# Kernel tuning notes

Hardware: AMD Instinct MI355X
Metric: run time of the kernel (lower is better)

## Reference

```python
import jax, jax.numpy as jnp
import numpy as np

H = 64   # hidden size
V = 29   # vocab / feature size
SOS = 27 # start-token index set to 1 in the initial one-hot


def _cell(x, h, c, Wih, Whh, bih, bhh):
    # PyTorch LSTMCell gate order: i, f, g, o
    g = x @ Wih.T + h @ Whh.T + bih + bhh
    i, f, gg, o = jnp.split(g, 4, axis=-1)
    c = jax.nn.sigmoid(f) * c + jax.nn.sigmoid(i) * jnp.tanh(gg)
    h = jax.nn.sigmoid(o) * jnp.tanh(c)
    return h, c


def setup_inputs() -> dict:
    key = jax.random.key(0)
    ks = iter(jax.random.split(key, 32))
    T, B = 1024, 512
    def p(shape, scale=0.05):
        return jax.random.normal(next(ks), shape, dtype=jnp.float32) * scale
    inp = {"input_seq": jax.random.normal(next(ks), (T, B, V), dtype=jnp.float32)}
    inp.update(
        enc_Wih0=p((4 * H, V)), enc_Whh0=p((4 * H, H)), enc_bih0=p((4 * H,)), enc_bhh0=p((4 * H,)),
        enc_Wih1=p((4 * H, H)), enc_Whh1=p((4 * H, H)), enc_bih1=p((4 * H,)), enc_bhh1=p((4 * H,)),
        d1_Wih=p((4 * H, V)), d1_Whh=p((4 * H, H)), d1_bih=p((4 * H,)), d1_bhh=p((4 * H,)),
        d2_Wih=p((4 * H, H)), d2_Whh=p((4 * H, H)), d2_bih=p((4 * H,)), d2_bhh=p((4 * H,)),
        cls_W=p((V, H)), cls_b=p((V,)),
    )
    return inp


def reference(input_seq, enc_Wih0, enc_Whh0, enc_bih0, enc_bhh0,
              enc_Wih1, enc_Whh1, enc_bih1, enc_bhh1,
              d1_Wih, d1_Whh, d1_bih, d1_bhh,
              d2_Wih, d2_Whh, d2_bih, d2_bhh,
              cls_W, cls_b):
    T, B, _ = input_seq.shape
    dt = input_seq.dtype
    z = jnp.zeros((B, H), dt)

    def layer(x_seq, Wih, Whh, bih, bhh):
        def step(carry, x):
            h, c = _cell(x, carry[0], carry[1], Wih, Whh, bih, bhh)
            return (h, c), h
        (h, c), ys = jax.lax.scan(step, (z, z), x_seq)
        return ys, h, c

    # 2-layer encoder LSTM with zero initial state
    y1, _, _ = layer(input_seq, enc_Wih0, enc_Whh0, enc_bih0, enc_bhh0)
    _, h1, c1 = layer(y1, enc_Wih1, enc_Whh1, enc_bih1, enc_bhh1)  # top-layer final (h, c)

    let0 = jnp.zeros((B, V), dt).at[:, SOS].set(1.0)

    def dec_step(carry, _):
        h1, c1, h2, c2, let = carry
        h1, c1 = _cell(let, h1, c1, d1_Wih, d1_Whh, d1_bih, d1_bhh)
        h2, c2 = _cell(h1, h2, c2, d2_Wih, d2_Whh, d2_bih, d2_bhh)
        pred = h2 @ cls_W.T + cls_b  # [B, V]
        idx = jnp.argmax(pred, axis=-1)  # [B]
        # Faithful to original bug: sets column idx[b] to 1 for ALL rows, for each b
        let = jnp.zeros((B, V), pred.dtype).at[:, idx].set(1.0)
        return (h1, c1, h2, c2, let), pred

    _, outputs = jax.lax.scan(dec_step, (h1, c1, z, z, let0), None, length=T)
    return outputs  # [T, B, V]
```

## Files before the change

kernel.cpp:

```cpp
#include <hip/hip_runtime.h>
#include <math.h>

#define TSTEPS 1024
#define BATCH  512
#define HID    64
#define VOC    29
#define SOS    27
#define MASK29 0x1FFFFFFFu

#define ENC_BLOCKS 256
#define DEC_BLOCKS 256
#define NTHREADS   512

__device__ __forceinline__ float frcp(float x){ return __builtin_amdgcn_rcpf(x); }
__device__ __forceinline__ float sigmf(float x){ return frcp(1.0f + __expf(-x)); }
__device__ __forceinline__ float tanhfast(float x){ return 1.0f - 2.0f*frcp(1.0f + __expf(2.0f*x)); }

__global__ __attribute__((amdgpu_flat_work_group_size(NTHREADS,NTHREADS), amdgpu_waves_per_eu(2,2)))
void enc_kernel(const float* __restrict__ x,
                const float* __restrict__ Wih0, const float* __restrict__ Whh0,
                const float* __restrict__ bih0, const float* __restrict__ bhh0,
                const float* __restrict__ Wih1, const float* __restrict__ Whh1,
                const float* __restrict__ bih1, const float* __restrict__ bhh1,
                float* __restrict__ h1g, float* __restrict__ c1g)
{
  const int tid = threadIdx.x;
  const int b0  = blockIdx.x * 2;
  const bool g0 = tid < 256;
  const int  r  = g0 ? tid : (tid-256);

  __shared__ __align__(16) float xs[2][32];
  __shared__ __align__(16) float h0s[2][HID], h1s[2][HID];
  __shared__ __align__(16) float gA[2][256], gB[2][256];

  float wh[64], w2[64];
  if (g0){
    #pragma unroll
    for (int k=0;k<64;k++) wh[k] = Whh0[r*64+k];
    #pragma unroll
    for (int k=0;k<29;k++) w2[k] = Wih0[r*29+k];
    #pragma unroll
    for (int k=29;k<64;k++) w2[k] = 0.f;
  } else {
    #pragma unroll
    for (int k=0;k<64;k++){ wh[k] = Whh1[r*64+k]; w2[k] = Wih1[r*64+k]; }
  }
  const float bias = g0 ? (bih0[r]+bhh0[r]) : (bih1[r]+bhh1[r]);

  float creg = 0.f;
  if (tid < 128){ int u=tid>>6,k=tid&63; h0s[u][k]=0.f; h1s[u][k]=0.f; }

  const int pidx = tid - 448;
  const bool pf  = (pidx >= 0) && (pidx < 2*VOC);
  const int prow = pf ? (pidx/VOC) : 0;
  const int pcol = pf ? (pidx%VOC) : 0;
  if (pf) xs[prow][pcol] = x[(size_t)(b0+prow)*VOC + pcol];
  __syncthreads();

  for (int t=0;t<=TSTEPS;t++){
    float xv = 0.f;
    if (pf && t+1 < TSTEPS)
      xv = x[(size_t)(t+1)*BATCH*VOC + (size_t)(b0+prow)*VOC + pcol];

    if (g0){
      if (t < TSTEPS){
        #pragma unroll
        for (int u=0;u<2;u++){
          float a0=bias,a1=0.f,a2=0.f,a3=0.f;
          const float4* xv4 = (const float4*)xs[u];
          #pragma unroll
          for (int c=0;c<7;c++){
            float4 q=xv4[c];
            a0=fmaf(q.x,w2[4*c+0],a0); a1=fmaf(q.y,w2[4*c+1],a1);
            a2=fmaf(q.z,w2[4*c+2],a2); a3=fmaf(q.w,w2[4*c+3],a3);
          }
          a0=fmaf(xs[u][28],w2[28],a0);
          const float4* h4=(const float4*)h0s[u];
          #pragma unroll
          for (int c=0;c<16;c++){
            float4 q=h4[c];
            a0=fmaf(q.x,wh[4*c+0],a0); a1=fmaf(q.y,wh[4*c+1],a1);
            a2=fmaf(q.z,wh[4*c+2],a2); a3=fmaf(q.w,wh[4*c+3],a3);
          }
          gA[u][r]=(a0+a1)+(a2+a3);
        }
      }
    } else {
      if (t >= 1){
        #pragma unroll
        for (int u=0;u<2;u++){
          float a0=bias,a1=0.f,a2=0.f,a3=0.f;
          const float4* i4=(const float4*)h0s[u];
          const float4* h4=(const float4*)h1s[u];
          #pragma unroll
          for (int c=0;c<16;c++){
            float4 q=i4[c], w=h4[c];
            a0=fmaf(q.x,w2[4*c+0],a0); a1=fmaf(q.y,w2[4*c+1],a1);
            a2=fmaf(q.z,w2[4*c+2],a2); a3=fmaf(q.w,w2[4*c+3],a3);
            a0=fmaf(w.x,wh[4*c+0],a0); a1=fmaf(w.y,wh[4*c+1],a1);
            a2=fmaf(w.z,wh[4*c+2],a2); a3=fmaf(w.w,wh[4*c+3],a3);
          }
          gB[u][r]=(a0+a1)+(a2+a3);
        }
      }
    }
    __syncthreads();
    if (tid < 128){
      if (t < TSTEPS){
        int u=tid>>6,k=tid&63;
        float ig=gA[u][k],fg=gA[u][64+k],gg=gA[u][128+k],og=gA[u][192+k];
        float c=sigmf(fg)*creg + sigmf(ig)*tanhfast(gg);
        creg=c; h0s[u][k]=sigmf(og)*tanhfast(c);
      }
    } else if (tid < 384){
      if (t >= 1){
        int tt=tid-256,u=tt>>6,k=tt&63;
        float ig=gB[u][k],fg=gB[u][64+k],gg=gB[u][128+k],og=gB[u][192+k];
        float c=sigmf(fg)*creg + sigmf(ig)*tanhfast(gg);
        creg=c; h1s[u][k]=sigmf(og)*tanhfast(c);
      }
    }
    if (pf && t+1 < TSTEPS) xs[prow][pcol] = xv;
    __syncthreads();
  }

  if (tid >= 256 && tid < 384){
    int tt=tid-256,u=tt>>6,k=tt&63;
    h1g[(b0+u)*HID+k]=h1s[u][k];
    c1g[(b0+u)*HID+k]=creg;
  }
}

__global__ __attribute__((amdgpu_flat_work_group_size(NTHREADS,NTHREADS), amdgpu_waves_per_eu(2,2)))
void dec_kernel(const float* __restrict__ h1gp, const float* __restrict__ c1gp,
                const float* __restrict__ W1ih, const float* __restrict__ W1hh,
                const float* __restrict__ b1ih, const float* __restrict__ b1hh,
                const float* __restrict__ W2ih, const float* __restrict__ W2hh,
                const float* __restrict__ b2ih, const float* __restrict__ b2hh,
                const float* __restrict__ clsW, const float* __restrict__ clsb,
                float* __restrict__ out,
                unsigned long long* __restrict__ lvl1)
{
  const int tid  = threadIdx.x;
  const int r    = tid >> 1;
  const int p    = tid & 1;
  const int b0   = blockIdx.x * 2;
  const unsigned grp = blockIdx.x & 15;
  const unsigned idx = blockIdx.x >> 4;

  __shared__ __align__(16) float clsW_s[VOC][68];
  __shared__ __align__(16) float clsb_s[32];
  __shared__ __align__(16) float gl[2][256];
  __shared__ __align__(16) float h1s[2][HID], h2s[2][HID];
  __shared__ unsigned maskLDS;

  for (int i=tid;i<VOC*HID;i+=NTHREADS) clsW_s[i/HID][i%HID] = clsW[i];
  if (tid<VOC) clsb_s[tid]=clsb[tid];

  float w1h[32], w2i[32], w2h[32], wi1c[15];
  #pragma unroll
  for (int k=0;k<32;k++){
    w1h[k]=W1hh[r*HID+32*p+k];
    w2i[k]=W2ih[r*HID+32*p+k];
    w2h[k]=W2hh[r*HID+32*p+k];
  }
  const int cbase = p ? 15 : 0;
  const int cn    = p ? 14 : 15;
  #pragma unroll
  for (int j=0;j<15;j++) wi1c[j] = (j<cn) ? W1ih[r*VOC+cbase+j] : 0.f;
  const float biasg = p ? 0.f : (b1ih[r]+b1hh[r]);
  const float bias2 = p ? 0.f : (b2ih[r]+b2hh[r]);

  float c1reg=0.f, c2reg=0.f;
  if (tid<128){
    int u=tid>>6,k=tid&63;
    h1s[u][k]=h1gp[(b0+u)*HID+k];
    c1reg    =c1gp[(b0+u)*HID+k];
    h2s[u][k]=0.f;
  }
  __syncthreads();

  float hd1[2];
  #pragma unroll
  for (int u=0;u<2;u++){
    float a0=0.f,a1=0.f,a2=0.f,a3=0.f;
    const float4* h4=(const float4*)(h1s[u]+32*p);
    #pragma unroll
    for (int c=0;c<8;c++){
      float4 q=h4[c];
      a0=fmaf(q.x,w1h[4*c+0],a0); a1=fmaf(q.y,w1h[4*c+1],a1);
      a2=fmaf(q.z,w1h[4*c+2],a2); a3=fmaf(q.w,w1h[4*c+3],a3);
    }
    hd1[u]=(a0+a1)+(a2+a3);
  }

  unsigned mask = 1u<<SOS;

  for (int s=0;s<TSTEPS;s++){
    #pragma unroll
    for (int u=0;u<2;u++){
      float it = biasg;
      #pragma unroll
      for (int j=0;j<15;j++)
        it += ((mask>>(cbase+j))&1u) ? wi1c[j] : 0.f;
      float v = it + hd1[u];
      v += __shfl_xor(v,1);
      if (!p) gl[u][r] = v;
    }
    __syncthreads();
    if (tid<128){
      int u=tid>>6,k=tid&63;
      float ig=gl[u][k],fg=gl[u][64+k],gg=gl[u][128+k],og=gl[u][192+k];
      float c=sigmf(fg)*c1reg+sigmf(ig)*tanhfast(gg);
      c1reg=c; h1s[u][k]=sigmf(og)*tanhfast(c);
    }
    __syncthreads();
    #pragma unroll
    for (int u=0;u<2;u++){
      float a0=bias2,a1=0.f,a2=0.f,a3=0.f;
      const float4* i4=(const float4*)(h1s[u]+32*p);
      const float4* h4=(const float4*)(h2s[u]+32*p);
      #pragma unroll
      for (int c=0;c<8;c++){
        float4 q=i4[c], w=h4[c];
        a0=fmaf(q.x,w2i[4*c+0],a0); a1=fmaf(q.y,w2i[4*c+1],a1);
        a2=fmaf(q.z,w2i[4*c+2],a2); a3=fmaf(q.w,w2i[4*c+3],a3);
        a0=fmaf(w.x,w2h[4*c+0],a0); a1=fmaf(w.y,w2h[4*c+1],a1);
        a2=fmaf(w.z,w2h[4*c+2],a2); a3=fmaf(w.w,w2h[4*c+3],a3);
      }
      float v=(a0+a1)+(a2+a3);
      v += __shfl_xor(v,1);
      if (!p) gl[u][r]=v;
    }
    __syncthreads();
    if (tid<128){
      int u=tid>>6,k=tid&63;
      float ig=gl[u][k],fg=gl[u][64+k],gg=gl[u][128+k],og=gl[u][192+k];
      float c=sigmf(fg)*c2reg+sigmf(ig)*tanhfast(gg);
      c2reg=c; h2s[u][k]=sigmf(og)*tanhfast(c);
    }
    __syncthreads();
    if (tid<64){
      int row=tid>>5, v=tid&31;
      float pv = -INFINITY;
      if (v<VOC){
        float a0=clsb_s[v],a1=0.f,a2=0.f,a3=0.f;
        const float4* h4=(const float4*)h2s[row];
        #pragma unroll
        for (int c=0;c<16;c++){
          float4 q=h4[c];
          a0=fmaf(q.x,clsW_s[v][4*c+0],a0); a1=fmaf(q.y,clsW_s[v][4*c+1],a1);
          a2=fmaf(q.z,clsW_s[v][4*c+2],a2); a3=fmaf(q.w,clsW_s[v][4*c+3],a3);
        }
        pv=(a0+a1)+(a2+a3);
        out[((size_t)s*BATCH + (size_t)(b0+row))*VOC + v]=pv;
      }
      int ix=v;
      #pragma unroll
      for (int off=16; off>0; off>>=1){
        float ov=__shfl_xor(pv,off);
        int   oi=__shfl_xor(ix,off);
        if (ov>pv || (ov==pv && oi<ix)){ pv=ov; ix=oi; }
      }
      unsigned bit = 1u<<ix;
      unsigned mb  = bit | __shfl_xor(bit,32);
      if (tid==0 && s+1<TSTEPS)
        __hip_atomic_fetch_or(&lvl1[(size_t)grp*TSTEPS+s],
                              (unsigned long long)mb | (1ULL<<(32+idx)),
                              __ATOMIC_RELAXED, __HIP_MEMORY_SCOPE_AGENT);
    }
    if (s+1<TSTEPS){
      #pragma unroll
      for (int u=0;u<2;u++){
        float a0=0.f,a1=0.f,a2=0.f,a3=0.f;
        const float4* h4=(const float4*)(h1s[u]+32*p);
        #pragma unroll
        for (int c=0;c<8;c++){
          float4 q=h4[c];
          a0=fmaf(q.x,w1h[4*c+0],a0); a1=fmaf(q.y,w1h[4*c+1],a1);
          a2=fmaf(q.z,w1h[4*c+2],a2); a3=fmaf(q.w,w1h[4*c+3],a3);
        }
        hd1[u]=(a0+a1)+(a2+a3);
      }
      if (tid<64){
        while (true){
          unsigned long long u64 = 0;
          if (tid<16)
            u64 = __hip_atomic_load(&lvl1[(size_t)tid*TSTEPS+s],
                                    __ATOMIC_RELAXED, __HIP_MEMORY_SCOPE_AGENT);
          bool ok = (tid>=16) || ((unsigned)(u64>>32) == 0xFFFFu);
          if (__ballot(ok) == ~0ull){
            unsigned m = (tid<16) ? ((unsigned)u64 & MASK29) : 0u;
            m |= __shfl_xor(m,1); m |= __shfl_xor(m,2);
            m |= __shfl_xor(m,4); m |= __shfl_xor(m,8);
            if (tid==0) maskLDS = m;
            break;
          }
        }
      }
      __syncthreads();
      mask = maskLDS;
    }
  }
}

extern "C" void kernel_launch(void* const* d_in, const int* in_sizes, int n_in,
                              void* d_out, int out_size, void* d_ws, size_t ws_size,
                              hipStream_t stream)
{
  const float* x     = (const float*)d_in[0];
  const float* eWih0 = (const float*)d_in[1];
  const float* eWhh0 = (const float*)d_in[2];
  const float* ebih0 = (const float*)d_in[3];
  const float* ebhh0 = (const float*)d_in[4];
  const float* eWih1 = (const float*)d_in[5];
  const float* eWhh1 = (const float*)d_in[6];
  const float* ebih1 = (const float*)d_in[7];
  const float* ebhh1 = (const float*)d_in[8];
  const float* d1Wih = (const float*)d_in[9];
  const float* d1Whh = (const float*)d_in[10];
  const float* d1bih = (const float*)d_in[11];
  const float* d1bhh = (const float*)d_in[12];
  const float* d2Wih = (const float*)d_in[13];
  const float* d2Whh = (const float*)d_in[14];
  const float* d2bih = (const float*)d_in[15];
  const float* d2bhh = (const float*)d_in[16];
  const float* clsW  = (const float*)d_in[17];
  const float* clsb  = (const float*)d_in[18];
  float* out = (float*)d_out;

  float* h1g = (float*)d_ws;
  float* c1g = h1g + BATCH*HID;
  unsigned long long* lvl1 = (unsigned long long*)((char*)d_ws + (size_t)(2*BATCH*HID)*sizeof(float));

  hipMemsetAsync(lvl1, 0, 16*TSTEPS*sizeof(unsigned long long), stream);

  enc_kernel<<<ENC_BLOCKS, NTHREADS, 0, stream>>>(
      x, eWih0,eWhh0,ebih0,ebhh0, eWih1,eWhh1,ebih1,ebhh1, h1g,c1g);

  void* args[] = { (void*)&h1g, (void*)&c1g,
                   (void*)&d1Wih,(void*)&d1Whh,(void*)&d1bih,(void*)&d1bhh,
                   (void*)&d2Wih,(void*)&d2Whh,(void*)&d2bih,(void*)&d2bhh,
                   (void*)&clsW,(void*)&clsb,(void*)&out,(void*)&lvl1 };
  hipLaunchCooperativeKernel((void*)dec_kernel, dim3(DEC_BLOCKS), dim3(NTHREADS),
                             args, 0, stream);
}
```

Before: 5.881 ms.

## Remap decoder threads so gate octets compute cell update via shuffles

Decoder threads are remapped so that the 8 lanes handling one hidden unit hold all four gate rows (i,f,g,o) split in halves. After a pairwise shuffle reduction, lane 0 of each octet gathers the other gates by xor-shuffles and updates the cell directly, which removes the shared gate buffer and two block barriers per step. The h1/h2 shared buffers are double-buffered to avoid read/write hazards, and an s_sleep is added in the spin-wait loop to reduce polling pressure. The cell update now runs on 1 of every 8 lanes and c state is replicated in registers.

```diff
diff --git a/kernel.cpp b/kernel.cpp
--- a/kernel.cpp
+++ b/kernel.cpp
@@ -141,42 +141,43 @@
                 float* __restrict__ out,
                 unsigned long long* __restrict__ lvl1)
 {
-  const int tid  = threadIdx.x;
-  const int r    = tid >> 1;
-  const int p    = tid & 1;
-  const int b0   = blockIdx.x * 2;
+  const int tid = threadIdx.x;
+  const int k   = tid >> 3;
+  const int l   = tid & 7;
+  const int g   = l >> 1;
+  const int p   = l & 1;
+  const int b0  = blockIdx.x * 2;
   const unsigned grp = blockIdx.x & 15;
   const unsigned idx = blockIdx.x >> 4;
+  const int row = g*64 + k;
 
   __shared__ __align__(16) float clsW_s[VOC][68];
   __shared__ __align__(16) float clsb_s[32];
-  __shared__ __align__(16) float gl[2][256];
-  __shared__ __align__(16) float h1s[2][HID], h2s[2][HID];
+  __shared__ __align__(16) float h1s[2][2][HID], h2s[2][2][HID];
   __shared__ unsigned maskLDS;
 
-  for (int i=tid;i<VOC*HID;i+=NTHREADS) clsW_s[i/HID][i%HID] = clsW[i];
+  for (int i=tid;i<VOC*HID;i+=NTHREADS) clsW_s[i/HID][i%HID]=clsW[i];
   if (tid<VOC) clsb_s[tid]=clsb[tid];
 
-  float w1h[32], w2i[32], w2h[32], wi1c[15];
+  float wi1c[15], w1h[32], w2i[32], w2h[32];
   #pragma unroll
-  for (int k=0;k<32;k++){
-    w1h[k]=W1hh[r*HID+32*p+k];
-    w2i[k]=W2ih[r*HID+32*p+k];
-    w2h[k]=W2hh[r*HID+32*p+k];
-  }
-  const int cbase = p ? 15 : 0;
-  const int cn    = p ? 14 : 15;
+  for (int j=0;j<15;j++) wi1c[j] = (p && j==14) ? 0.f : W1ih[row*VOC + p*15 + j];
   #pragma unroll
-  for (int j=0;j<15;j++) wi1c[j] = (j<cn) ? W1ih[r*VOC+cbase+j] : 0.f;
-  const float biasg = p ? 0.f : (b1ih[r]+b1hh[r]);
-  const float bias2 = p ? 0.f : (b2ih[r]+b2hh[r]);
-
-  float c1reg=0.f, c2reg=0.f;
+  for (int j=0;j<32;j++){
+    w1h[j]=W1hh[row*HID+32*p+j];
+    w2i[j]=W2ih[row*HID+32*p+j];
+    w2h[j]=W2hh[row*HID+32*p+j];
+  }
+  const float bs1 = p?0.f:(b1ih[row]+b1hh[row]);
+  const float bs2 = p?0.f:(b2ih[row]+b2hh[row]);
+
+  float c1[2], c2[2]={0.f,0.f};
+  #pragma unroll
+  for (int u=0;u<2;u++) c1[u] = c1gp[(b0+u)*HID+k];
   if (tid<128){
-    int u=tid>>6,k=tid&63;
-    h1s[u][k]=h1gp[(b0+u)*HID+k];
-    c1reg    =c1gp[(b0+u)*HID+k];
-    h2s[u][k]=0.f;
+    int uu=tid>>6,kk=tid&63;
+    h1s[1][uu][kk]=h1gp[(b0+uu)*HID+kk];
+    h2s[1][uu][kk]=0.f;
   }
   __syncthreads();
 
@@ -184,10 +185,10 @@
   #pragma unroll
   for (int u=0;u<2;u++){
     float a0=0.f,a1=0.f,a2=0.f,a3=0.f;
-    const float4* h4=(const float4*)(h1s[u]+32*p);
+    const float4* hv=(const float4*)&h1s[1][u][32*p];
     #pragma unroll
     for (int c=0;c<8;c++){
-      float4 q=h4[c];
+      float4 q=hv[c];
       a0=fmaf(q.x,w1h[4*c+0],a0); a1=fmaf(q.y,w1h[4*c+1],a1);
       a2=fmaf(q.z,w1h[4*c+2],a2); a3=fmaf(q.w,w1h[4*c+3],a3);
     }
@@ -197,32 +198,34 @@
   unsigned mask = 1u<<SOS;
 
   for (int s=0;s<TSTEPS;s++){
+    const int wb=s&1, rb=wb^1;
+
     #pragma unroll
     for (int u=0;u<2;u++){
-      float it = biasg;
+      float v = hd1[u] + bs1;
       #pragma unroll
       for (int j=0;j<15;j++)
-        it += ((mask>>(cbase+j))&1u) ? wi1c[j] : 0.f;
-      float v = it + hd1[u];
+        v += ((mask>>(p*15+j))&1u) ? wi1c[j] : 0.f;
       v += __shfl_xor(v,1);
-      if (!p) gl[u][r] = v;
+      float fv = __shfl_xor(v,2);
+      float gv = __shfl_xor(v,4);
+      float ov = __shfl_xor(v,6);
+      if (l==0){
+        float c=sigmf(fv)*c1[u] + sigmf(v)*tanhfast(gv);
+        c1[u]=c;
+        h1s[wb][u][k]=sigmf(ov)*tanhfast(c);
+      }
     }
     __syncthreads();
-    if (tid<128){
-      int u=tid>>6,k=tid&63;
-      float ig=gl[u][k],fg=gl[u][64+k],gg=gl[u][128+k],og=gl[u][192+k];
-      float c=sigmf(fg)*c1reg+sigmf(ig)*tanhfast(gg);
-      c1reg=c; h1s[u][k]=sigmf(og)*tanhfast(c);
-    }
-    __syncthreads();
+
     #pragma unroll
     for (int u=0;u<2;u++){
-      float a0=bias2,a1=0.f,a2=0.f,a3=0.f;
-      const float4* i4=(const float4*)(h1s[u]+32*p);
-      const float4* h4=(const float4*)(h2s[u]+32*p);
+      float a0=bs2,a1=0.f,a2=0.f,a3=0.f;
+      const float4* iv=(const float4*)&h1s[wb][u][32*p];
+      const float4* hv=(const float4*)&h2s[rb][u][32*p];
       #pragma unroll
       for (int c=0;c<8;c++){
-        float4 q=i4[c], w=h4[c];
+        float4 q=iv[c], w=hv[c];
         a0=fmaf(q.x,w2i[4*c+0],a0); a1=fmaf(q.y,w2i[4*c+1],a1);
         a2=fmaf(q.z,w2i[4*c+2],a2); a3=fmaf(q.w,w2i[4*c+3],a3);
         a0=fmaf(w.x,w2h[4*c+0],a0); a1=fmaf(w.y,w2h[4*c+1],a1);
@@ -230,32 +233,33 @@
       }
       float v=(a0+a1)+(a2+a3);
       v += __shfl_xor(v,1);
-      if (!p) gl[u][r]=v;
+      float fv = __shfl_xor(v,2);
+      float gv = __shfl_xor(v,4);
+      float ov = __shfl_xor(v,6);
+      if (l==0){
+        float c=sigmf(fv)*c2[u] + sigmf(v)*tanhfast(gv);
+        c2[u]=c;
+        h2s[wb][u][k]=sigmf(ov)*tanhfast(c);
+      }
     }
     __syncthreads();
-    if (tid<128){
-      int u=tid>>6,k=tid&63;
-      float ig=gl[u][k],fg=gl[u][64+k],gg=gl[u][128+k],og=gl[u][192+k];
-      float c=sigmf(fg)*c2reg+sigmf(ig)*tanhfast(gg);
-      c2reg=c; h2s[u][k]=sigmf(og)*tanhfast(c);
-    }
-    __syncthreads();
+
     if (tid<64){
-      int row=tid>>5, v=tid&31;
-      float pv = -INFINITY;
-      if (v<VOC){
-        float a0=clsb_s[v],a1=0.f,a2=0.f,a3=0.f;
-        const float4* h4=(const float4*)h2s[row];
+      int row2=tid>>5, v2=tid&31;
+      float pv=-INFINITY;
+      if (v2<VOC){
+        float a0=clsb_s[v2],a1=0.f,a2=0.f,a3=0.f;
+        const float4* h4=(const float4*)h2s[wb][row2];
         #pragma unroll
         for (int c=0;c<16;c++){
           float4 q=h4[c];
-          a0=fmaf(q.x,clsW_s[v][4*c+0],a0); a1=fmaf(q.y,clsW_s[v][4*c+1],a1);
-          a2=fmaf(q.z,clsW_s[v][4*c+2],a2); a3=fmaf(q.w,clsW_s[v][4*c+3],a3);
+          a0=fmaf(q.x,clsW_s[v2][4*c+0],a0); a1=fmaf(q.y,clsW_s[v2][4*c+1],a1);
+          a2=fmaf(q.z,clsW_s[v2][4*c+2],a2); a3=fmaf(q.w,clsW_s[v2][4*c+3],a3);
         }
         pv=(a0+a1)+(a2+a3);
-        out[((size_t)s*BATCH + (size_t)(b0+row))*VOC + v]=pv;
-      }
-      int ix=v;
+        out[((size_t)s*BATCH + (size_t)(b0+row2))*VOC + v2]=pv;
+      }
+      int ix=v2;
       #pragma unroll
       for (int off=16; off>0; off>>=1){
         float ov=__shfl_xor(pv,off);
@@ -269,19 +273,19 @@
                               (unsigned long long)mb | (1ULL<<(32+idx)),
                               __ATOMIC_RELAXED, __HIP_MEMORY_SCOPE_AGENT);
     }
+    #pragma unroll
+    for (int u=0;u<2;u++){
+      float a0=0.f,a1=0.f,a2=0.f,a3=0.f;
+      const float4* hv=(const float4*)&h1s[wb][u][32*p];
+      #pragma unroll
+      for (int c=0;c<8;c++){
+        float4 q=hv[c];
+        a0=fmaf(q.x,w1h[4*c+0],a0); a1=fmaf(q.y,w1h[4*c+1],a1);
+        a2=fmaf(q.z,w1h[4*c+2],a2); a3=fmaf(q.w,w1h[4*c+3],a3);
+      }
+      hd1[u]=(a0+a1)+(a2+a3);
+    }
     if (s+1<TSTEPS){
-      #pragma unroll
-      for (int u=0;u<2;u++){
-        float a0=0.f,a1=0.f,a2=0.f,a3=0.f;
-        const float4* h4=(const float4*)(h1s[u]+32*p);
-        #pragma unroll
-        for (int c=0;c<8;c++){
-          float4 q=h4[c];
-          a0=fmaf(q.x,w1h[4*c+0],a0); a1=fmaf(q.y,w1h[4*c+1],a1);
-          a2=fmaf(q.z,w1h[4*c+2],a2); a3=fmaf(q.w,w1h[4*c+3],a3);
-        }
-        hd1[u]=(a0+a1)+(a2+a3);
-      }
       if (tid<64){
         while (true){
           unsigned long long u64 = 0;
@@ -296,6 +300,7 @@
             if (tid==0) maskLDS = m;
             break;
           }
+          __builtin_amdgcn_s_sleep(1);
         }
       }
       __syncthreads();
```

Result: slower. 6.576 ms (+11.8%).
